# Performance work log

Hardware: AMD Instinct MI355X
Metric: run time of the kernel (lower is better)

The kernel has to match this reference:

```python
import jax, jax.numpy as jnp
import numpy as np

N, D_IN, D_OUT, N_CTRS, K = 16384, 64, 64, 512, 16


def setup_inputs() -> dict:
    key = jax.random.key(0)
    k1, k2, k3, k4 = jax.random.split(key, 4)
    x = jax.random.normal(k1, (N, D_IN), dtype=jnp.float32)
    ctrs = jax.random.normal(k2, (N_CTRS, D_IN), dtype=jnp.float32)
    Wv = jax.random.normal(k3, (N_CTRS, D_IN, D_OUT), dtype=jnp.float32) * 0.02
    Ov = jax.random.normal(k4, (N_CTRS, D_OUT), dtype=jnp.float32) * 0.02
    return {"x": x, "ctrs": ctrs, "Wv": Wv, "Ov": Ov, "k": K}


def reference(x, ctrs, Wv, Ov, k):
    n = x.shape[0]
    # squared distances via expansion (same math as sum((x-c)^2), avoids [n,C,d] blowup)
    x2 = jnp.sum(x * x, axis=1, keepdims=True)            # [n,1]
    c2 = jnp.sum(ctrs * ctrs, axis=1)                     # [C]
    dist_sq = x2 + c2[None, :] - 2.0 * (x @ ctrs.T)       # [n,C]
    # k nearest centers; softmax over negative squared distances of the k selected
    neg_top, idx = jax.lax.top_k(-dist_sq, k)             # [n,k] each
    scores = jax.nn.softmax(neg_top, axis=1)              # [n,k]
    # dense soft-assignment matrix (only k nonzeros per row), as in the torch code
    A = jnp.zeros_like(dist_sq).at[jnp.arange(n)[:, None], idx].set(scores)  # [n,C]
    # per-token affine mix: sum_c A[n,c] * (x[n] @ Wv[c] + Ov[c])
    scored_weights = jnp.einsum('nc,cgp->ngp', A, Wv)     # [n,d_in,d_out]
    out = jnp.einsum('ngp,ng->np', scored_weights, x) + A @ Ov  # [n,d_out]
    return out
```

## Files before the change

kernel.cpp:

```cpp
#include <hip/hip_runtime.h>

#define N_TOK 16384
#define D 64
#define NC 512
#define KSEL 16
#define NPAIR (N_TOK * KSEL)
#define PADCAP 327168

typedef __attribute__((ext_vector_type(8))) short short8;
typedef __attribute__((ext_vector_type(16))) float float16;

__device__ __forceinline__ unsigned fkey(float f) {
    unsigned u = __float_as_uint(f);
    return (u & 0x80000000u) ? ~u : (u | 0x80000000u);
}
__device__ __forceinline__ float funkey(unsigned k) {
    unsigned u = (k & 0x80000000u) ? (k & 0x7fffffffu) : ~k;
    return __uint_as_float(u);
}
__device__ __forceinline__ unsigned short bfr(float f) {
    unsigned u = __float_as_uint(f);
    return (unsigned short)((u + 0x7FFFu + ((u >> 16) & 1u)) >> 16);
}
__device__ __forceinline__ float b2f(unsigned short h) {
    return __uint_as_float((unsigned)h << 16);
}
__device__ __forceinline__ unsigned pk2(unsigned short a, unsigned short b) {
    return (unsigned)a | ((unsigned)b << 16);
}

__device__ __forceinline__ void ins16(unsigned (&run)[16], unsigned k) {
    #pragma unroll
    for (int r = 0; r < 16; ++r) {
        unsigned mx = run[r] > k ? run[r] : k;
        unsigned mn = run[r] > k ? k : run[r];
        run[r] = mx; k = mn;
    }
}

__global__ __launch_bounds__(256, 3) void topk13_kernel(
    const float* __restrict__ x, const float* __restrict__ ctrs,
    unsigned* __restrict__ pk) {
    __shared__ __align__(16) unsigned char pool[35328];
    unsigned short* Cbf = (unsigned short*)pool;
    unsigned* Sbk = (unsigned*)pool;
    unsigned* mbp = (unsigned*)pool;
    float* c2s = (float*)(pool + 34816);

    const int t = threadIdx.x;
    const int lane = t & 63;
    const int wv = t >> 6;
    const int mrow = lane & 31;
    const int half = lane >> 5;
    const int tb = blockIdx.x >> 2;
    const int p = blockIdx.x & 3;
    const int base = tb * 128;
    const int cbase = p * 128;

    {
        const int r = t >> 1, q = t & 1;
        const float4* cp = (const float4*)(ctrs + (cbase + r) * D + q * 32);
        unsigned short* Ch = Cbf + r * 136 + q * 32;
        float s2 = 0.f;
        #pragma unroll
        for (int i = 0; i < 8; ++i) {
            float4 v = cp[i];
            s2 += v.x * v.x + v.y * v.y + v.z * v.z + v.w * v.w;
            unsigned short h0 = bfr(v.x), h1 = bfr(v.y), h2 = bfr(v.z), h3 = bfr(v.w);
            unsigned short l0 = bfr(v.x - b2f(h0)), l1 = bfr(v.y - b2f(h1));
            unsigned short l2 = bfr(v.z - b2f(h2)), l3 = bfr(v.w - b2f(h3));
            *(uint2*)(Ch + 4 * i)      = make_uint2(pk2(h0, h1), pk2(h2, h3));
            *(uint2*)(Ch + 64 + 4 * i) = make_uint2(pk2(l0, l1), pk2(l2, l3));
        }
        s2 += __shfl_xor(s2, 1);
        c2s[r] = s2;
    }

    short8 ah[4], al[4];
    {
        const float* xp = x + (base + wv * 32 + mrow) * D + half * 8;
        #pragma unroll
        for (int kt = 0; kt < 4; ++kt) {
            float4 u = *(const float4*)(xp + kt * 16);
            float4 v = *(const float4*)(xp + kt * 16 + 4);
            float c[8] = {u.x, u.y, u.z, u.w, v.x, v.y, v.z, v.w};
            #pragma unroll
            for (int j = 0; j < 8; ++j) {
                unsigned short h = bfr(c[j]);
                ah[kt][j] = (short)h;
                al[kt][j] = (short)bfr(c[j] - b2f(h));
            }
        }
    }
    __syncthreads();

    float16 acc0 = {0.f,0.f,0.f,0.f,0.f,0.f,0.f,0.f,0.f,0.f,0.f,0.f,0.f,0.f,0.f,0.f};
    float16 acc1 = acc0, acc2 = acc0, acc3 = acc0;

    const unsigned short* Bbase = Cbf + mrow * 136 + half * 8;
    #pragma unroll
    for (int kt = 0; kt < 4; ++kt) {
        const unsigned short* Bp = Bbase + kt * 16;
        short8 b0 = *(const short8*)(Bp);
        short8 b1 = *(const short8*)(Bp + 32 * 136);
        short8 b2 = *(const short8*)(Bp + 64 * 136);
        short8 b3 = *(const short8*)(Bp + 96 * 136);
        acc0 = __builtin_amdgcn_mfma_f32_32x32x16_bf16(ah[kt], b0, acc0, 0, 0, 0);
        acc1 = __builtin_amdgcn_mfma_f32_32x32x16_bf16(ah[kt], b1, acc1, 0, 0, 0);
        acc2 = __builtin_amdgcn_mfma_f32_32x32x16_bf16(ah[kt], b2, acc2, 0, 0, 0);
        acc3 = __builtin_amdgcn_mfma_f32_32x32x16_bf16(ah[kt], b3, acc3, 0, 0, 0);
        acc0 = __builtin_amdgcn_mfma_f32_32x32x16_bf16(al[kt], b0, acc0, 0, 0, 0);
        acc1 = __builtin_amdgcn_mfma_f32_32x32x16_bf16(al[kt], b1, acc1, 0, 0, 0);
        acc2 = __builtin_amdgcn_mfma_f32_32x32x16_bf16(al[kt], b2, acc2, 0, 0, 0);
        acc3 = __builtin_amdgcn_mfma_f32_32x32x16_bf16(al[kt], b3, acc3, 0, 0, 0);
        b0 = *(const short8*)(Bp + 64);
        b1 = *(const short8*)(Bp + 64 + 32 * 136);
        b2 = *(const short8*)(Bp + 64 + 64 * 136);
        b3 = *(const short8*)(Bp + 64 + 96 * 136);
        acc0 = __builtin_amdgcn_mfma_f32_32x32x16_bf16(ah[kt], b0, acc0, 0, 0, 0);
        acc1 = __builtin_amdgcn_mfma_f32_32x32x16_bf16(ah[kt], b1, acc1, 0, 0, 0);
        acc2 = __builtin_amdgcn_mfma_f32_32x32x16_bf16(ah[kt], b2, acc2, 0, 0, 0);
        acc3 = __builtin_amdgcn_mfma_f32_32x32x16_bf16(ah[kt], b3, acc3, 0, 0, 0);
    }
    __syncthreads();

    unsigned run[16];
    #pragma unroll
    for (int r = 0; r < 16; ++r) run[r] = 0u;

    const int tok = t & 127;
    const int h = t >> 7;

    {
        float ca = c2s[mrow];
        float cb = c2s[32 + mrow];
        #pragma unroll
        for (int reg = 0; reg < 16; ++reg) {
            int tokrow = wv * 32 + (reg & 3) + 8 * (reg >> 2) + 4 * half;
            float sa = fmaf(2.f, acc0[reg], -ca);
            float sb = fmaf(2.f, acc1[reg], -cb);
            Sbk[tokrow * 68 + mrow]      = (fkey(sa) & 0xFFFFFE00u) | (unsigned)(cbase + mrow);
            Sbk[tokrow * 68 + 32 + mrow] = (fkey(sb) & 0xFFFFFE00u) | (unsigned)(cbase + 32 + mrow);
        }
    }
    __syncthreads();
    #pragma unroll
    for (int i = 0; i < 8; ++i) {
        uint4 kv = *(const uint4*)(Sbk + tok * 68 + h * 32 + 4 * ((i + tok) & 7));
        ins16(run, kv.x); ins16(run, kv.y); ins16(run, kv.z); ins16(run, kv.w);
    }
    __syncthreads();

    {
        float ca = c2s[64 + mrow];
        float cb = c2s[96 + mrow];
        #pragma unroll
        for (int reg = 0; reg < 16; ++reg) {
            int tokrow = wv * 32 + (reg & 3) + 8 * (reg >> 2) + 4 * half;
            float sa = fmaf(2.f, acc2[reg], -ca);
            float sb = fmaf(2.f, acc3[reg], -cb);
            Sbk[tokrow * 68 + mrow]      = (fkey(sa) & 0xFFFFFE00u) | (unsigned)(cbase + 64 + mrow);
            Sbk[tokrow * 68 + 32 + mrow] = (fkey(sb) & 0xFFFFFE00u) | (unsigned)(cbase + 96 + mrow);
        }
    }
    __syncthreads();
    #pragma unroll
    for (int i = 0; i < 8; ++i) {
        uint4 kv = *(const uint4*)(Sbk + tok * 68 + h * 32 + 4 * ((i + tok) & 7));
        ins16(run, kv.x); ins16(run, kv.y); ins16(run, kv.z); ins16(run, kv.w);
    }
    __syncthreads();

    #pragma unroll
    for (int r = 0; r < 16; ++r) mbp[tok * 33 + h * 16 + r] = run[r];
    __syncthreads();

    if (t < 128) {
        const unsigned* A = mbp + t * 33;
        const unsigned* B = A + 16;
        unsigned m[16];
        int ia = 0, ib = 0;
        unsigned va = A[0], vb = B[0];
        #pragma unroll
        for (int r = 0; r < 16; ++r) {
            bool ta = va > vb;
            m[r] = ta ? va : vb;
            if (ta) { ++ia; va = (ia < 16) ? A[ia] : 0u; }
            else    { ++ib; vb = (ib < 16) ? B[ib] : 0u; }
        }
        uint4* dst = (uint4*)(pk + (size_t)(base + t) * 64 + p * 16);
        dst[0] = make_uint4(m[0], m[1], m[2], m[3]);
        dst[1] = make_uint4(m[4], m[5], m[6], m[7]);
        dst[2] = make_uint4(m[8], m[9], m[10], m[11]);
        dst[3] = make_uint4(m[12], m[13], m[14], m[15]);
    }
}

__global__ __launch_bounds__(256) void topmerge_kernel(
    const unsigned* __restrict__ pk, float* __restrict__ scores,
    int* __restrict__ sidx, int* __restrict__ hist) {
    __shared__ int lhist[NC];
    const int t = threadIdx.x;
    lhist[t] = 0; lhist[t + 256] = 0;
    __syncthreads();
    const int n = blockIdx.x * 256 + t;
    const unsigned* p = pk + (size_t)n * 64;
    unsigned h[4]; int pos[4];
    #pragma unroll
    for (int w = 0; w < 4; ++w) { pos[w] = 0; h[w] = p[w * 16]; }
    float vals[16]; int ids[16];
    #pragma unroll
    for (int r = 0; r < KSEL; ++r) {
        unsigned m = h[0];
        #pragma unroll
        for (int w = 1; w < 4; ++w) m = m > h[w] ? m : h[w];
        vals[r] = funkey(m);
        ids[r] = (int)(m & 511u);
        #pragma unroll
        for (int w = 0; w < 4; ++w) {
            if (h[w] == m) {
                ++pos[w];
                h[w] = (pos[w] < KSEL) ? p[w * 16 + pos[w]] : 0u;
            }
        }
    }
    float mx = vals[0];
    float e[16]; float sum = 0.f;
    #pragma unroll
    for (int r = 0; r < KSEL; ++r) { e[r] = __expf(vals[r] - mx); sum += e[r]; }
    float inv = 1.f / sum;
    #pragma unroll
    for (int q = 0; q < 4; ++q) {
        *(float4*)(scores + n * KSEL + 4 * q) =
            make_float4(e[4*q] * inv, e[4*q+1] * inv, e[4*q+2] * inv, e[4*q+3] * inv);
        *(int4*)(sidx + n * KSEL + 4 * q) =
            make_int4(ids[4*q], ids[4*q+1], ids[4*q+2], ids[4*q+3]);
    }
    #pragma unroll
    for (int r = 0; r < KSEL; ++r) atomicAdd(&lhist[ids[r]], 1);
    __syncthreads();
    { int hv = lhist[t]; if (hv) atomicAdd(&hist[t], hv); }
    { int hv = lhist[t + 256]; if (hv) atomicAdd(&hist[t + 256], hv); }
}

__global__ __launch_bounds__(512) void scan2_kernel(const int* __restrict__ hist,
                                                    int* __restrict__ cursor,
                                                    int* __restrict__ meta) {
    __shared__ int buf[2][NC];
    int t = threadIdx.x;
    int pad = (hist[t] + 127) & ~127;
    buf[0][t] = pad;
    __syncthreads();
    int a = 0;
    for (int d = 1; d < NC; d <<= 1) {
        int val = buf[a][t] + (t >= d ? buf[a][t - d] : 0);
        buf[1 - a][t] = val;
        __syncthreads();
        a = 1 - a;
    }
    int incl = buf[a][t];
    cursor[t] = incl - pad;
    if (t == NC - 1) meta[0] = incl;
}

__global__ __launch_bounds__(256) void scatter4_kernel(
    const int* __restrict__ sidx, const float* __restrict__ scores,
    int* __restrict__ cursor, int* __restrict__ tokentab,
    float* __restrict__ scotab) {
    __shared__ int lh[NC];
    __shared__ int lbase[NC];
    const int t = threadIdx.x;
    for (int i = t; i < NC; i += 256) lh[i] = 0;
    __syncthreads();
    const int base_e = blockIdx.x * 1024;
    int myc[4];
    #pragma unroll
    for (int i = 0; i < 4; ++i) {
        int c = sidx[base_e + t + 256 * i];
        myc[i] = c;
        atomicAdd(&lh[c], 1);
    }
    __syncthreads();
    for (int i = t; i < NC; i += 256) {
        int h = lh[i];
        lbase[i] = h ? atomicAdd(&cursor[i], h) : 0;
        lh[i] = 0;
    }
    __syncthreads();
    #pragma unroll
    for (int i = 0; i < 4; ++i) {
        int e = base_e + t + 256 * i;
        int c = myc[i];
        int pos = lbase[c] + atomicAdd(&lh[c], 1);
        tokentab[pos] = (c << 19) | e;
        scotab[pos] = scores[e];
    }
}

__global__ __launch_bounds__(256) void mix15_kernel(
    const float* __restrict__ x, const float* __restrict__ Wv,
    const float* __restrict__ Ov, const int* __restrict__ tokentab,
    const float* __restrict__ scotab, const int* __restrict__ meta,
    float* __restrict__ partial) {
    __shared__ __align__(16) unsigned short Wt[64 * 72];
    __shared__ int eT[128];
    __shared__ float sT[128];

    const int t = threadIdx.x;
    const int base = blockIdx.x * 128;
    if (base >= meta[0]) return;

    const int c = (int)(((unsigned)tokentab[base]) >> 19);

    {
        const float* Wp = Wv + c * (D * D) + (t & 63);
        const int gb = (t >> 6) * 16;
        #pragma unroll
        for (int g = 0; g < 16; g += 2) {
            float v0 = Wp[(gb + g) * 64];
            float v1 = Wp[(gb + g + 1) * 64];
            unsigned pkw = (unsigned)bfr(v0) | ((unsigned)bfr(v1) << 16);
            *(unsigned*)&Wt[(t & 63) * 72 + gb + g] = pkw;
        }
    }
    if (t < 128) {
        unsigned w = (unsigned)tokentab[base + t];
        eT[t] = (int)(w & 0x7FFFFu);
        sT[t] = scotab[base + t];
    }
    __syncthreads();

    const int lane = t & 63;
    const int wv = t >> 6;
    const int mrow = lane & 31;
    const int half = lane >> 5;
    const int row = wv * 32 + mrow;

    const int   mye = eT[row];
    const int   myn = (mye < NPAIR) ? (mye >> 4) : 0;
    const float mys = sT[row];

    const float* xp = x + myn * D + half * 8;
    float4 f[8];
    #pragma unroll
    for (int kt = 0; kt < 4; ++kt) {
        f[2 * kt]     = *(const float4*)(xp + kt * 16);
        f[2 * kt + 1] = *(const float4*)(xp + kt * 16 + 4);
    }
    short8 a[4];
    #pragma unroll
    for (int kt = 0; kt < 4; ++kt) {
        float4 u = f[2 * kt], v = f[2 * kt + 1];
        a[kt][0] = (short)bfr(u.x * mys); a[kt][1] = (short)bfr(u.y * mys);
        a[kt][2] = (short)bfr(u.z * mys); a[kt][3] = (short)bfr(u.w * mys);
        a[kt][4] = (short)bfr(v.x * mys); a[kt][5] = (short)bfr(v.y * mys);
        a[kt][6] = (short)bfr(v.z * mys); a[kt][7] = (short)bfr(v.w * mys);
    }

    float16 acc0 = {0.f,0.f,0.f,0.f,0.f,0.f,0.f,0.f,0.f,0.f,0.f,0.f,0.f,0.f,0.f,0.f};
    float16 acc1 = {0.f,0.f,0.f,0.f,0.f,0.f,0.f,0.f,0.f,0.f,0.f,0.f,0.f,0.f,0.f,0.f};

    const unsigned short* B0 = Wt + mrow * 72;
    const unsigned short* B1 = Wt + (mrow + 32) * 72;
    #pragma unroll
    for (int kt = 0; kt < 4; ++kt) {
        short8 b0 = *(const short8*)(B0 + kt * 16 + half * 8);
        short8 b1 = *(const short8*)(B1 + kt * 16 + half * 8);
        acc0 = __builtin_amdgcn_mfma_f32_32x32x16_bf16(a[kt], b0, acc0, 0, 0, 0);
        acc1 = __builtin_amdgcn_mfma_f32_32x32x16_bf16(a[kt], b1, acc1, 0, 0, 0);
    }

    const float ov0 = Ov[c * D + mrow];
    const float ov1 = Ov[c * D + 32 + mrow];
    #pragma unroll
    for (int reg = 0; reg < 16; ++reg) {
        int orow = wv * 32 + (reg & 3) + 8 * (reg >> 2) + 4 * half;
        float s = sT[orow];
        int e = eT[orow];
        if (e < NPAIR) {
            float* dst = partial + (size_t)e * D;
            dst[mrow]      = acc0[reg] + s * ov0;
            dst[32 + mrow] = acc1[reg] + s * ov1;
        }
    }
}

__global__ __launch_bounds__(256) void redu_kernel(
    const float* __restrict__ partial, float* __restrict__ out) {
    const int g = blockIdx.x * 256 + threadIdx.x;
    const int n = g >> 4;
    const int d4 = (g & 15) * 4;
    const float* p = partial + (size_t)n * (KSEL * D) + d4;
    float4 s = make_float4(0.f, 0.f, 0.f, 0.f);
    #pragma unroll
    for (int r = 0; r < KSEL; ++r) {
        float4 v = *(const float4*)(p + r * D);
        s.x += v.x; s.y += v.y; s.z += v.z; s.w += v.w;
    }
    *(float4*)(out + n * D + d4) = s;
}

__global__ __launch_bounds__(256) void mix14_kernel(
    const float* __restrict__ x, const float* __restrict__ Wv,
    const float* __restrict__ Ov, const int* __restrict__ tokentab,
    const float* __restrict__ scotab, const int* __restrict__ meta,
    float* __restrict__ out) {
    __shared__ __align__(16) unsigned short Wt[64 * 72];
    __shared__ int tT[128];
    __shared__ float sT[128];

    const int t = threadIdx.x;
    const int base = blockIdx.x * 128;
    if (base >= meta[0]) return;

    const int c = (int)(((unsigned)tokentab[base]) >> 19);

    {
        const float* Wp = Wv + c * (D * D) + (t & 63);
        const int gb = (t >> 6) * 16;
        #pragma unroll
        for (int g = 0; g < 16; g += 2) {
            float v0 = Wp[(gb + g) * 64];
            float v1 = Wp[(gb + g + 1) * 64];
            unsigned pkw = (unsigned)bfr(v0) | ((unsigned)bfr(v1) << 16);
            *(unsigned*)&Wt[(t & 63) * 72 + gb + g] = pkw;
        }
    }
    if (t < 128) {
        unsigned w = (unsigned)tokentab[base + t];
        tT[t] = (int)((w & 0x7FFFFu) >> 4);
        sT[t] = scotab[base + t];
    }
    __syncthreads();

    const int lane = t & 63;
    const int wv = t >> 6;
    const int mrow = lane & 31;
    const int half = lane >> 5;
    const int row = wv * 32 + mrow;

    const int   myn = tT[row];
    const float mys = sT[row];

    const float* xp = x + myn * D + half * 8;
    float4 f[8];
    #pragma unroll
    for (int kt = 0; kt < 4; ++kt) {
        f[2 * kt]     = *(const float4*)(xp + kt * 16);
        f[2 * kt + 1] = *(const float4*)(xp + kt * 16 + 4);
    }
    short8 a[4];
    #pragma unroll
    for (int kt = 0; kt < 4; ++kt) {
        float4 u = f[2 * kt], v = f[2 * kt + 1];
        a[kt][0] = (short)bfr(u.x * mys); a[kt][1] = (short)bfr(u.y * mys);
        a[kt][2] = (short)bfr(u.z * mys); a[kt][3] = (short)bfr(u.w * mys);
        a[kt][4] = (short)bfr(v.x * mys); a[kt][5] = (short)bfr(v.y * mys);
        a[kt][6] = (short)bfr(v.z * mys); a[kt][7] = (short)bfr(v.w * mys);
    }

    float16 acc0 = {0.f,0.f,0.f,0.f,0.f,0.f,0.f,0.f,0.f,0.f,0.f,0.f,0.f,0.f,0.f,0.f};
    float16 acc1 = {0.f,0.f,0.f,0.f,0.f,0.f,0.f,0.f,0.f,0.f,0.f,0.f,0.f,0.f,0.f,0.f};

    const unsigned short* B0 = Wt + mrow * 72;
    const unsigned short* B1 = Wt + (mrow + 32) * 72;
    #pragma unroll
    for (int kt = 0; kt < 4; ++kt) {
        short8 b0 = *(const short8*)(B0 + kt * 16 + half * 8);
        short8 b1 = *(const short8*)(B1 + kt * 16 + half * 8);
        acc0 = __builtin_amdgcn_mfma_f32_32x32x16_bf16(a[kt], b0, acc0, 0, 0, 0);
        acc1 = __builtin_amdgcn_mfma_f32_32x32x16_bf16(a[kt], b1, acc1, 0, 0, 0);
    }

    const float ov0 = Ov[c * D + mrow];
    const float ov1 = Ov[c * D + 32 + mrow];
    #pragma unroll
    for (int reg = 0; reg < 16; ++reg) {
        int orow = wv * 32 + (reg & 3) + 8 * (reg >> 2) + 4 * half;
        float s = sT[orow];
        if (s != 0.f) {
            int n = tT[orow];
            unsafeAtomicAdd(out + n * D + mrow,      acc0[reg] + s * ov0);
            unsafeAtomicAdd(out + n * D + 32 + mrow, acc1[reg] + s * ov1);
        }
    }
}

extern "C" void kernel_launch(void* const* d_in, const int* in_sizes, int n_in,
                              void* d_out, int out_size, void* d_ws, size_t ws_size,
                              hipStream_t stream) {
    const float* x    = (const float*)d_in[0];
    const float* ctrs = (const float*)d_in[1];
    const float* Wv   = (const float*)d_in[2];
    const float* Ov   = (const float*)d_in[3];
    float* out = (float*)d_out;

    int*   hist     = (int*)d_ws + 512;
    int*   meta     = (int*)d_ws + 1024;
    int*   cursor   = (int*)d_ws + 2048;
    float* scores   = (float*)d_ws + 2560;
    int*   sidx     = (int*)d_ws + 2560 + NPAIR;
    int*   tokentab = (int*)d_ws + 2560 + 2 * NPAIR;
    float* scotab   = (float*)d_ws + 2560 + 2 * NPAIR + PADCAP;
    float* partial  = (float*)d_ws + 2560 + 2 * NPAIR + 2 * PADCAP;
    unsigned* pkbuf = (unsigned*)partial;

    const size_t need = ((size_t)2560 + 2 * (size_t)NPAIR + 2 * (size_t)PADCAP) * 4
                      + (size_t)NPAIR * D * 4;
    const bool fast = ws_size >= need;

    hipMemsetAsync(hist, 0, NC * sizeof(int), stream);
    hipMemsetAsync(scotab, 0, (size_t)PADCAP * sizeof(float), stream);
    if (fast) {
        hipMemsetAsync(tokentab, 0xFF, (size_t)PADCAP * sizeof(int), stream);
    } else {
        hipMemsetAsync(out, 0, (size_t)N_TOK * D * sizeof(float), stream);
        hipMemsetAsync(tokentab, 0, (size_t)PADCAP * sizeof(int), stream);
    }
    hipLaunchKernelGGL(topk13_kernel, dim3((N_TOK / 128) * 4), dim3(256), 0, stream,
                       x, ctrs, pkbuf);
    hipLaunchKernelGGL(topmerge_kernel, dim3(N_TOK / 256), dim3(256), 0, stream,
                       pkbuf, scores, sidx, hist);
    hipLaunchKernelGGL(scan2_kernel, dim3(1), dim3(512), 0, stream, hist, cursor, meta);
    hipLaunchKernelGGL(scatter4_kernel, dim3(256), dim3(256), 0, stream,
                       sidx, scores, cursor, tokentab, scotab);
    if (fast) {
        hipLaunchKernelGGL(mix15_kernel, dim3(PADCAP / 128), dim3(256), 0, stream,
                           x, Wv, Ov, tokentab, scotab, meta, partial);
        hipLaunchKernelGGL(redu_kernel, dim3(NPAIR / 256), dim3(256), 0, stream,
                           partial, out);
    } else {
        hipLaunchKernelGGL(mix14_kernel, dim3(PADCAP / 128), dim3(256), 0, stream,
                           x, Wv, Ov, tokentab, scotab, meta, out);
    }
}
```

Before: 153.3 us.

## Retile top-k to 64 tokens, store partials in fp16, drop scotab memset

The distance/top-k kernel now handles 64 tokens per block, with each wave computing a 32x64 tile. It runs a single shared-memory pass with a swizzled read pattern and a 4-way merge, and its launch bound is raised to 4 blocks per unit. The per-pair partial outputs are stored as fp16 instead of fp32, which halves the write and read traffic of the mix and reduce stages; the reduce kernel now handles 8 halves per thread. The scotab memset is skipped on the fast path. The fp16 partials lose precision and may risk tolerance.

```diff
diff --git a/kernel.cpp b/kernel.cpp
--- a/kernel.cpp
+++ b/kernel.cpp
@@ -1,4 +1,5 @@
 #include <hip/hip_runtime.h>
+#include <hip/hip_fp16.h>
 
 #define N_TOK 16384
 #define D 64
@@ -8,6 +9,7 @@
 #define PADCAP 327168
 
 typedef __attribute__((ext_vector_type(8))) short short8;
+typedef __attribute__((ext_vector_type(8))) unsigned short ushort8;
 typedef __attribute__((ext_vector_type(16))) float float16;
 
 __device__ __forceinline__ unsigned fkey(float f) {
@@ -38,7 +40,7 @@
     }
 }
 
-__global__ __launch_bounds__(256, 3) void topk13_kernel(
+__global__ __launch_bounds__(256, 4) void topk14_kernel(
     const float* __restrict__ x, const float* __restrict__ ctrs,
     unsigned* __restrict__ pk) {
     __shared__ __align__(16) unsigned char pool[35328];
@@ -54,8 +56,10 @@
     const int half = lane >> 5;
     const int tb = blockIdx.x >> 2;
     const int p = blockIdx.x & 3;
-    const int base = tb * 128;
+    const int base = tb * 64;
     const int cbase = p * 128;
+    const int trow = (wv & 1) * 32;
+    const int cgrp = (wv >> 1) * 64;
 
     {
         const int r = t >> 1, q = t & 1;
@@ -78,7 +82,7 @@
 
     short8 ah[4], al[4];
     {
-        const float* xp = x + (base + wv * 32 + mrow) * D + half * 8;
+        const float* xp = x + (base + trow + mrow) * D + half * 8;
         #pragma unroll
         for (int kt = 0; kt < 4; ++kt) {
             float4 u = *(const float4*)(xp + kt * 16);
@@ -95,104 +99,88 @@
     __syncthreads();
 
     float16 acc0 = {0.f,0.f,0.f,0.f,0.f,0.f,0.f,0.f,0.f,0.f,0.f,0.f,0.f,0.f,0.f,0.f};
-    float16 acc1 = acc0, acc2 = acc0, acc3 = acc0;
-
-    const unsigned short* Bbase = Cbf + mrow * 136 + half * 8;
-    #pragma unroll
-    for (int kt = 0; kt < 4; ++kt) {
-        const unsigned short* Bp = Bbase + kt * 16;
-        short8 b0 = *(const short8*)(Bp);
-        short8 b1 = *(const short8*)(Bp + 32 * 136);
-        short8 b2 = *(const short8*)(Bp + 64 * 136);
-        short8 b3 = *(const short8*)(Bp + 96 * 136);
-        acc0 = __builtin_amdgcn_mfma_f32_32x32x16_bf16(ah[kt], b0, acc0, 0, 0, 0);
-        acc1 = __builtin_amdgcn_mfma_f32_32x32x16_bf16(ah[kt], b1, acc1, 0, 0, 0);
-        acc2 = __builtin_amdgcn_mfma_f32_32x32x16_bf16(ah[kt], b2, acc2, 0, 0, 0);
-        acc3 = __builtin_amdgcn_mfma_f32_32x32x16_bf16(ah[kt], b3, acc3, 0, 0, 0);
-        acc0 = __builtin_amdgcn_mfma_f32_32x32x16_bf16(al[kt], b0, acc0, 0, 0, 0);
-        acc1 = __builtin_amdgcn_mfma_f32_32x32x16_bf16(al[kt], b1, acc1, 0, 0, 0);
-        acc2 = __builtin_amdgcn_mfma_f32_32x32x16_bf16(al[kt], b2, acc2, 0, 0, 0);
-        acc3 = __builtin_amdgcn_mfma_f32_32x32x16_bf16(al[kt], b3, acc3, 0, 0, 0);
-        b0 = *(const short8*)(Bp + 64);
-        b1 = *(const short8*)(Bp + 64 + 32 * 136);
-        b2 = *(const short8*)(Bp + 64 + 64 * 136);
-        b3 = *(const short8*)(Bp + 64 + 96 * 136);
-        acc0 = __builtin_amdgcn_mfma_f32_32x32x16_bf16(ah[kt], b0, acc0, 0, 0, 0);
-        acc1 = __builtin_amdgcn_mfma_f32_32x32x16_bf16(ah[kt], b1, acc1, 0, 0, 0);
-        acc2 = __builtin_amdgcn_mfma_f32_32x32x16_bf16(ah[kt], b2, acc2, 0, 0, 0);
-        acc3 = __builtin_amdgcn_mfma_f32_32x32x16_bf16(ah[kt], b3, acc3, 0, 0, 0);
-    }
-    __syncthreads();
-
-    unsigned run[16];
-    #pragma unroll
-    for (int r = 0; r < 16; ++r) run[r] = 0u;
-
-    const int tok = t & 127;
-    const int h = t >> 7;
+    float16 acc1 = acc0;
+
+    const unsigned short* B0 = Cbf + (cgrp + mrow) * 136 + half * 8;
+    const unsigned short* B1 = Cbf + (cgrp + 32 + mrow) * 136 + half * 8;
+    #pragma unroll
+    for (int kt = 0; kt < 4; ++kt) {
+        short8 bh0 = *(const short8*)(B0 + kt * 16);
+        short8 bh1 = *(const short8*)(B1 + kt * 16);
+        short8 bl0 = *(const short8*)(B0 + 64 + kt * 16);
+        short8 bl1 = *(const short8*)(B1 + 64 + kt * 16);
+        acc0 = __builtin_amdgcn_mfma_f32_32x32x16_bf16(ah[kt], bh0, acc0, 0, 0, 0);
+        acc1 = __builtin_amdgcn_mfma_f32_32x32x16_bf16(ah[kt], bh1, acc1, 0, 0, 0);
+        acc0 = __builtin_amdgcn_mfma_f32_32x32x16_bf16(al[kt], bh0, acc0, 0, 0, 0);
+        acc1 = __builtin_amdgcn_mfma_f32_32x32x16_bf16(al[kt], bh1, acc1, 0, 0, 0);
+        acc0 = __builtin_amdgcn_mfma_f32_32x32x16_bf16(ah[kt], bl0, acc0, 0, 0, 0);
+        acc1 = __builtin_amdgcn_mfma_f32_32x32x16_bf16(ah[kt], bl1, acc1, 0, 0, 0);
+    }
+    __syncthreads();
 
     {
-        float ca = c2s[mrow];
-        float cb = c2s[32 + mrow];
+        float ca = c2s[cgrp + mrow];
+        float cb = c2s[cgrp + 32 + mrow];
         #pragma unroll
         for (int reg = 0; reg < 16; ++reg) {
-            int tokrow = wv * 32 + (reg & 3) + 8 * (reg >> 2) + 4 * half;
+            int tokrow = trow + (reg & 3) + 8 * (reg >> 2) + 4 * half;
             float sa = fmaf(2.f, acc0[reg], -ca);
             float sb = fmaf(2.f, acc1[reg], -cb);
-            Sbk[tokrow * 68 + mrow]      = (fkey(sa) & 0xFFFFFE00u) | (unsigned)(cbase + mrow);
-            Sbk[tokrow * 68 + 32 + mrow] = (fkey(sb) & 0xFFFFFE00u) | (unsigned)(cbase + 32 + mrow);
-        }
-    }
-    __syncthreads();
+            Sbk[tokrow * 132 + cgrp + mrow] =
+                (fkey(sa) & 0xFFFFFE00u) | (unsigned)(cbase + cgrp + mrow);
+            Sbk[tokrow * 132 + cgrp + 32 + mrow] =
+                (fkey(sb) & 0xFFFFFE00u) | (unsigned)(cbase + cgrp + 32 + mrow);
+        }
+    }
+    __syncthreads();
+
+    const int tok = t & 63;
+    const int h = t >> 6;
+    unsigned run[16];
+    #pragma unroll
+    for (int r = 0; r < 16; ++r) run[r] = 0u;
     #pragma unroll
     for (int i = 0; i < 8; ++i) {
-        uint4 kv = *(const uint4*)(Sbk + tok * 68 + h * 32 + 4 * ((i + tok) & 7));
+        int cq = ((i + tok) & 7) ^ ((tok >> 3) & 7);
+        uint4 kv = *(const uint4*)(Sbk + tok * 132 + 32 * h + 4 * cq);
         ins16(run, kv.x); ins16(run, kv.y); ins16(run, kv.z); ins16(run, kv.w);
     }
     __syncthreads();
 
     {
-        float ca = c2s[64 + mrow];
-        float cb = c2s[96 + mrow];
-        #pragma unroll
-        for (int reg = 0; reg < 16; ++reg) {
-            int tokrow = wv * 32 + (reg & 3) + 8 * (reg >> 2) + 4 * half;
-            float sa = fmaf(2.f, acc2[reg], -ca);
-            float sb = fmaf(2.f, acc3[reg], -cb);
-            Sbk[tokrow * 68 + mrow]      = (fkey(sa) & 0xFFFFFE00u) | (unsigned)(cbase + 64 + mrow);
-            Sbk[tokrow * 68 + 32 + mrow] = (fkey(sb) & 0xFFFFFE00u) | (unsigned)(cbase + 96 + mrow);
-        }
-    }
-    __syncthreads();
-    #pragma unroll
-    for (int i = 0; i < 8; ++i) {
-        uint4 kv = *(const uint4*)(Sbk + tok * 68 + h * 32 + 4 * ((i + tok) & 7));
-        ins16(run, kv.x); ins16(run, kv.y); ins16(run, kv.z); ins16(run, kv.w);
-    }
-    __syncthreads();
-
-    #pragma unroll
-    for (int r = 0; r < 16; ++r) mbp[tok * 33 + h * 16 + r] = run[r];
-    __syncthreads();
-
-    if (t < 128) {
-        const unsigned* A = mbp + t * 33;
-        const unsigned* B = A + 16;
-        unsigned m[16];
-        int ia = 0, ib = 0;
-        unsigned va = A[0], vb = B[0];
+        uint4* dst = (uint4*)(mbp + tok * 68 + h * 16);
+        dst[0] = make_uint4(run[0], run[1], run[2], run[3]);
+        dst[1] = make_uint4(run[4], run[5], run[6], run[7]);
+        dst[2] = make_uint4(run[8], run[9], run[10], run[11]);
+        dst[3] = make_uint4(run[12], run[13], run[14], run[15]);
+    }
+    __syncthreads();
+
+    if (t < 64) {
+        const unsigned* pm = mbp + t * 68;
+        unsigned hv[4]; int pos[4];
+        #pragma unroll
+        for (int w = 0; w < 4; ++w) { pos[w] = 0; hv[w] = pm[w * 16]; }
+        unsigned mm[16];
         #pragma unroll
         for (int r = 0; r < 16; ++r) {
-            bool ta = va > vb;
-            m[r] = ta ? va : vb;
-            if (ta) { ++ia; va = (ia < 16) ? A[ia] : 0u; }
-            else    { ++ib; vb = (ib < 16) ? B[ib] : 0u; }
+            unsigned m = hv[0];
+            #pragma unroll
+            for (int w = 1; w < 4; ++w) m = m > hv[w] ? m : hv[w];
+            mm[r] = m;
+            #pragma unroll
+            for (int w = 0; w < 4; ++w) {
+                if (hv[w] == m) {
+                    ++pos[w];
+                    hv[w] = (pos[w] < 16) ? pm[w * 16 + pos[w]] : 0u;
+                }
+            }
         }
         uint4* dst = (uint4*)(pk + (size_t)(base + t) * 64 + p * 16);
-        dst[0] = make_uint4(m[0], m[1], m[2], m[3]);
-        dst[1] = make_uint4(m[4], m[5], m[6], m[7]);
-        dst[2] = make_uint4(m[8], m[9], m[10], m[11]);
-        dst[3] = make_uint4(m[12], m[13], m[14], m[15]);
+        dst[0] = make_uint4(mm[0], mm[1], mm[2], mm[3]);
+        dst[1] = make_uint4(mm[4], mm[5], mm[6], mm[7]);
+        dst[2] = make_uint4(mm[8], mm[9], mm[10], mm[11]);
+        dst[3] = make_uint4(mm[12], mm[13], mm[14], mm[15]);
     }
 }
 
@@ -297,11 +285,11 @@
     }
 }
 
-__global__ __launch_bounds__(256) void mix15_kernel(
+__global__ __launch_bounds__(256) void mix16_kernel(
     const float* __restrict__ x, const float* __restrict__ Wv,
     const float* __restrict__ Ov, const int* __restrict__ tokentab,
     const float* __restrict__ scotab, const int* __restrict__ meta,
-    float* __restrict__ partial) {
+    __half* __restrict__ partial) {
     __shared__ __align__(16) unsigned short Wt[64 * 72];
     __shared__ int eT[128];
     __shared__ float sT[128];
@@ -378,26 +366,30 @@
         float s = sT[orow];
         int e = eT[orow];
         if (e < NPAIR) {
-            float* dst = partial + (size_t)e * D;
-            dst[mrow]      = acc0[reg] + s * ov0;
-            dst[32 + mrow] = acc1[reg] + s * ov1;
-        }
-    }
-}
-
-__global__ __launch_bounds__(256) void redu_kernel(
-    const float* __restrict__ partial, float* __restrict__ out) {
+            __half* dst = partial + (size_t)e * D;
+            dst[mrow]      = __float2half(acc0[reg] + s * ov0);
+            dst[32 + mrow] = __float2half(acc1[reg] + s * ov1);
+        }
+    }
+}
+
+__global__ __launch_bounds__(256) void redu2_kernel(
+    const __half* __restrict__ partial, float* __restrict__ out) {
     const int g = blockIdx.x * 256 + threadIdx.x;
-    const int n = g >> 4;
-    const int d4 = (g & 15) * 4;
-    const float* p = partial + (size_t)n * (KSEL * D) + d4;
-    float4 s = make_float4(0.f, 0.f, 0.f, 0.f);
+    const int n = g >> 3;
+    const int d8 = (g & 7) * 8;
+    const __half* p = partial + (size_t)n * (KSEL * D) + d8;
+    float s[8] = {0.f, 0.f, 0.f, 0.f, 0.f, 0.f, 0.f, 0.f};
     #pragma unroll
     for (int r = 0; r < KSEL; ++r) {
-        float4 v = *(const float4*)(p + r * D);
-        s.x += v.x; s.y += v.y; s.z += v.z; s.w += v.w;
-    }
-    *(float4*)(out + n * D + d4) = s;
+        ushort8 v = *(const ushort8*)(p + r * D);
+        #pragma unroll
+        for (int j = 0; j < 8; ++j)
+            s[j] += __half2float(__ushort_as_half((unsigned short)v[j]));
+    }
+    float* o = out + n * D + d8;
+    *(float4*)(o)     = make_float4(s[0], s[1], s[2], s[3]);
+    *(float4*)(o + 4) = make_float4(s[4], s[5], s[6], s[7]);
 }
 
 __global__ __launch_bounds__(256) void mix14_kernel(
@@ -502,22 +494,22 @@
     int*   sidx     = (int*)d_ws + 2560 + NPAIR;
     int*   tokentab = (int*)d_ws + 2560 + 2 * NPAIR;
     float* scotab   = (float*)d_ws + 2560 + 2 * NPAIR + PADCAP;
-    float* partial  = (float*)d_ws + 2560 + 2 * NPAIR + 2 * PADCAP;
+    __half* partial = (__half*)((int*)d_ws + 2560 + 2 * NPAIR + 2 * PADCAP);
     unsigned* pkbuf = (unsigned*)partial;
 
     const size_t need = ((size_t)2560 + 2 * (size_t)NPAIR + 2 * (size_t)PADCAP) * 4
-                      + (size_t)NPAIR * D * 4;
+                      + (size_t)NPAIR * D * 2;
     const bool fast = ws_size >= need;
 
     hipMemsetAsync(hist, 0, NC * sizeof(int), stream);
-    hipMemsetAsync(scotab, 0, (size_t)PADCAP * sizeof(float), stream);
     if (fast) {
         hipMemsetAsync(tokentab, 0xFF, (size_t)PADCAP * sizeof(int), stream);
     } else {
         hipMemsetAsync(out, 0, (size_t)N_TOK * D * sizeof(float), stream);
+        hipMemsetAsync(scotab, 0, (size_t)PADCAP * sizeof(float), stream);
         hipMemsetAsync(tokentab, 0, (size_t)PADCAP * sizeof(int), stream);
     }
-    hipLaunchKernelGGL(topk13_kernel, dim3((N_TOK / 128) * 4), dim3(256), 0, stream,
+    hipLaunchKernelGGL(topk14_kernel, dim3((N_TOK / 64) * 4), dim3(256), 0, stream,
                        x, ctrs, pkbuf);
     hipLaunchKernelGGL(topmerge_kernel, dim3(N_TOK / 256), dim3(256), 0, stream,
                        pkbuf, scores, sidx, hist);
@@ -525,9 +517,9 @@
     hipLaunchKernelGGL(scatter4_kernel, dim3(256), dim3(256), 0, stream,
                        sidx, scores, cursor, tokentab, scotab);
     if (fast) {
-        hipLaunchKernelGGL(mix15_kernel, dim3(PADCAP / 128), dim3(256), 0, stream,
+        hipLaunchKernelGGL(mix16_kernel, dim3(PADCAP / 128), dim3(256), 0, stream,
                            x, Wv, Ov, tokentab, scotab, meta, partial);
-        hipLaunchKernelGGL(redu_kernel, dim3(NPAIR / 256), dim3(256), 0, stream,
+        hipLaunchKernelGGL(redu2_kernel, dim3(N_TOK * 8 / 256), dim3(256), 0, stream,
                            partial, out);
     } else {
         hipLaunchKernelGGL(mix14_kernel, dim3(PADCAP / 128), dim3(256), 0, stream,
```

New measurement: 144.5 us. 1.06x faster.
